# Kernel optimization log

Measured on AMD Instinct MI355X. Metric: run time of the kernel, lower is better.

## Reference

```python
import jax, jax.numpy as jnp
import numpy as np


def setup_inputs() -> dict:
    key = jax.random.key(0)
    ks = jax.random.split(key, 8)
    B, C, H, W = 4, 256, 64, 64
    Ci = C // 8  # inter_channels = 32
    x = jax.random.normal(ks[0], (B, C, H, W), dtype=jnp.float32)
    # 1x1 conv weights stored as [out, in] matrices (kernel size 1)
    sq = 1.0 / np.sqrt(C)
    Wq = jax.random.uniform(ks[1], (Ci, C), jnp.float32, -sq, sq)
    bq = jax.random.uniform(ks[2], (Ci,), jnp.float32, -sq, sq)
    Wk = jax.random.uniform(ks[3], (Ci, C), jnp.float32, -sq, sq)
    bk = jax.random.uniform(ks[4], (Ci,), jnp.float32, -sq, sq)
    Wv = jax.random.uniform(ks[5], (C, C), jnp.float32, -sq, sq)
    bv = jax.random.uniform(ks[6], (C,), jnp.float32, -sq, sq)
    # torch initializes gamma to zeros; use a nonzero value so output depends on attention path
    gamma = jnp.array([0.5], dtype=jnp.float32)
    return {"x": x, "Wq": Wq, "bq": bq, "Wk": Wk, "bk": bk, "Wv": Wv, "bv": bv, "gamma": gamma}


def reference(x, Wq, bq, Wk, bk, Wv, bv, gamma):
    B, C, H, W = x.shape
    N = H * W
    xf = x.reshape(B, C, N)                        # [B, C, N]
    # 1x1 convs == channel-mixing matmuls
    q = jnp.einsum('oc,bcn->bon', Wq, xf) + bq[None, :, None]   # [B, Ci, N]
    k = jnp.einsum('oc,bcn->bon', Wk, xf) + bk[None, :, None]   # [B, Ci, N]
    v = jnp.einsum('oc,bcn->bon', Wv, xf) + bv[None, :, None]   # [B, C,  N]
    # energy[b, n, m] = sum_c q[b, c, n] * k[b, c, m]  (no scaling, per DANet)
    energy = jnp.einsum('bcn,bcm->bnm', q, k)      # [B, N, N]
    attention = jax.nn.softmax(energy, axis=-1)    # softmax over keys m
    # out[b, c, n] = sum_m v[b, c, m] * attention[b, n, m]
    out = jnp.einsum('bcm,bnm->bcn', v, attention)
    out = out.reshape(B, C, H, W)
    return gamma[0] * out + x
```

## Files before the change

### kernel.cpp

```cpp
#include <hip/hip_runtime.h>
#include <hip/hip_bf16.h>
#include <math.h>

typedef __bf16 bf16x8 __attribute__((ext_vector_type(8)));
typedef float  floatx4 __attribute__((ext_vector_type(4)));

#define MFMA(a, b, c) __builtin_amdgcn_mfma_f32_16x16x32_bf16((a), (b), (c), 0, 0, 0)

__device__ __forceinline__ unsigned short f2bf(float f) {
  union { float f; unsigned u; } v; v.f = f;
  unsigned r = v.u + 0x7FFFu + ((v.u >> 16) & 1u);
  return (unsigned short)(r >> 16);
}
__device__ __forceinline__ float bf2f(unsigned short u) {
  union { unsigned u; float f; } v; v.u = ((unsigned)u) << 16;
  return v.f;
}

__global__ __launch_bounds__(256) void k_wconv(const float* __restrict__ Wq,
                                               const float* __restrict__ Wk,
                                               const float* __restrict__ Wv,
                                               unsigned short* __restrict__ Wall) {
  int i = blockIdx.x * 256 + threadIdx.x;
  int o = i >> 8, c = i & 255;
  float v = (o < 32) ? Wq[o * 256 + c]
          : (o < 64) ? Wk[(o - 32) * 256 + c]
                     : Wv[(o - 64) * 256 + c];
  Wall[i] = f2bf(v);
}

__global__ __launch_bounds__(256) void k_xpose(const float* __restrict__ x,
                                               unsigned short* __restrict__ xT) {
  int bid = blockIdx.x;
  int b = bid >> 8, rem = bid & 255;
  int nb = rem >> 2, cb = rem & 3;
  int n0 = nb * 64, c0 = cb * 64;
  int tid = threadIdx.x;
  __shared__ alignas(16) unsigned short T[64][72];
#pragma unroll
  for (int i = 0; i < 4; ++i) {
    int idx = tid + 256 * i;
    int r = idx >> 4, g = idx & 15;
    float4 d = *(const float4*)(x + ((size_t)b * 256 + c0 + r) * 4096 + n0 + g * 4);
    T[g * 4 + 0][r] = f2bf(d.x);
    T[g * 4 + 1][r] = f2bf(d.y);
    T[g * 4 + 2][r] = f2bf(d.z);
    T[g * 4 + 3][r] = f2bf(d.w);
  }
  __syncthreads();
#pragma unroll
  for (int i = 0; i < 2; ++i) {
    int idx = tid + 256 * i;
    int j = idx >> 3, g = idx & 7;
    *(uint4*)(xT + ((size_t)b * 4096 + n0 + j) * 256 + c0 + g * 8) =
        *(const uint4*)&T[j][g * 8];
  }
}

__global__ __launch_bounds__(64, 4) void k_proj(const unsigned short* __restrict__ xT,
                                                const unsigned short* __restrict__ Wall,
                                                const float* __restrict__ bq,
                                                const float* __restrict__ bk,
                                                const float* __restrict__ bv,
                                                unsigned short* __restrict__ qkT,
                                                unsigned short* __restrict__ vbf) {
  int b = blockIdx.x >> 9;
  int m0 = ((blockIdx.x >> 1) & 255) * 16;
  int h = blockIdx.x & 1;
  int lane = threadIdx.x & 63;
  int l15 = lane & 15, quad = lane >> 4;

  floatx4 acc[10];
#pragma unroll
  for (int tt = 0; tt < 10; ++tt) acc[tt] = floatx4{0.f, 0.f, 0.f, 0.f};

  const unsigned short* arow = xT + ((size_t)b * 4096 + m0 + l15) * 256;
#pragma unroll
  for (int ks = 0; ks < 8; ++ks) {
    bf16x8 a = *(const bf16x8*)(arow + ks * 32 + quad * 8);
#pragma unroll
    for (int tt = 0; tt < 10; ++tt) {
      int gt = (tt < 2) ? (h * 2 + tt) : (4 + h * 8 + (tt - 2));
      bf16x8 w = *(const bf16x8*)(Wall + (size_t)(gt * 16 + l15) * 256 + ks * 32 + quad * 8);
      acc[tt] = MFMA(a, w, acc[tt]);
    }
  }
#pragma unroll
  for (int tt = 0; tt < 2; ++tt) {
    int o = (h * 2 + tt) * 16 + l15;
    float bias = (o < 32) ? bq[o] : bk[o - 32];
#pragma unroll
    for (int r = 0; r < 4; ++r) {
      int m = m0 + quad * 4 + r;
      qkT[((size_t)b * 4096 + m) * 64 + o] = f2bf(acc[tt][r] + bias);
    }
  }
  __shared__ alignas(16) unsigned short Os[128][24];
#pragma unroll
  for (int tt = 2; tt < 10; ++tt) {
    int lr = (tt - 2) * 16 + l15;
    int c = h * 128 + lr;
    float bias = bv[c];
#pragma unroll
    for (int r = 0; r < 4; ++r)
      Os[lr][quad * 4 + r] = f2bf(acc[tt][r] + bias);
  }
  __syncthreads();
#pragma unroll
  for (int i = 0; i < 4; ++i) {
    int idx = threadIdx.x + 64 * i;
    int r = idx >> 1, g = idx & 1;
    int c = h * 128 + r;
    *(uint4*)(vbf + ((size_t)b * 256 + c) * 4096 + m0 + g * 8) = *(const uint4*)&Os[r][g * 8];
  }
}

__global__ __launch_bounds__(256, 3) void k_attn(const unsigned short* __restrict__ qkT,
                                                 const unsigned short* __restrict__ vbf,
                                                 unsigned short* __restrict__ Obf,
                                                 float* __restrict__ lsum) {
  const int b = blockIdx.x >> 8;
  const int s = (blockIdx.x >> 6) & 3;
  const int q0 = (blockIdx.x & 63) * 64;
  const int tid = threadIdx.x;
  const int wave = tid >> 6, lane = tid & 63;
  const int l15 = lane & 15, quad = lane >> 4;

  __shared__ alignas(16) unsigned short Kl[2][64][40];
  __shared__ alignas(16) unsigned short Pl[4][16][72];

  bf16x8 aq = *(const bf16x8*)(qkT + ((size_t)b * 4096 + q0 + wave * 16 + l15) * 64 + quad * 8);

  floatx4 O[4][4];
#pragma unroll
  for (int qt = 0; qt < 4; ++qt)
#pragma unroll
    for (int nt = 0; nt < 4; ++nt) O[qt][nt] = floatx4{0.f, 0.f, 0.f, 0.f};

  float l_part = 0.f;
  const floatx4 zero4 = {0.f, 0.f, 0.f, 0.f};

  const unsigned short* vrow = vbf + ((size_t)b * 256 + wave * 64) * 4096;

  {
    int r = tid >> 2, g = tid & 3;
    uint4 d = *(const uint4*)(qkT + ((size_t)b * 4096 + s * 1024 + r) * 64 + 32 + g * 8);
    *(uint4*)&Kl[0][r][g * 8] = d;
  }
  __syncthreads();

  for (int it = 0; it < 16; ++it) {
    const int m0 = (s * 16 + it) * 64;
    const int buf = it & 1;

    bf16x8 vb[4][2];
#pragma unroll
    for (int nt = 0; nt < 4; ++nt)
#pragma unroll
      for (int kk = 0; kk < 2; ++kk)
        vb[nt][kk] = *(const bf16x8*)(vrow + (size_t)(nt * 16 + l15) * 4096 + m0 + kk * 32 + quad * 8);

    floatx4 st[4];
#pragma unroll
    for (int t = 0; t < 4; ++t) {
      bf16x8 kb = *(const bf16x8*)&Kl[buf][t * 16 + l15][quad * 8];
      st[t] = MFMA(kb, aq, zero4);
    }
#pragma unroll
    for (int t = 0; t < 4; ++t) {
      float p0 = __expf(st[t][0]);
      float p1 = __expf(st[t][1]);
      float p2 = __expf(st[t][2]);
      float p3 = __expf(st[t][3]);
      l_part += (p0 + p1) + (p2 + p3);
      ushort4 pk = make_ushort4(f2bf(p0), f2bf(p1), f2bf(p2), f2bf(p3));
      *(ushort4*)&Pl[wave][l15][t * 16 + quad * 4] = pk;
    }

    if (it < 15) {
      int r = tid >> 2, g = tid & 3;
      uint4 d = *(const uint4*)(qkT + ((size_t)b * 4096 + m0 + 64 + r) * 64 + 32 + g * 8);
      *(uint4*)&Kl[buf ^ 1][r][g * 8] = d;
    }
    __syncthreads();

#pragma unroll
    for (int qt = 0; qt < 4; ++qt) {
      bf16x8 pa0 = *(const bf16x8*)&Pl[qt][l15][quad * 8];
      bf16x8 pa1 = *(const bf16x8*)&Pl[qt][l15][32 + quad * 8];
#pragma unroll
      for (int nt = 0; nt < 4; ++nt) {
        O[qt][nt] = MFMA(pa0, vb[nt][0], O[qt][nt]);
        O[qt][nt] = MFMA(pa1, vb[nt][1], O[qt][nt]);
      }
    }
    __syncthreads();
  }

  float lt = l_part;
  lt += __shfl_xor(lt, 16);
  lt += __shfl_xor(lt, 32);
  if (quad == 0)
    lsum[((size_t)s * 4 + b) * 4096 + q0 + wave * 16 + l15] = lt;

#pragma unroll
  for (int nt = 0; nt < 4; ++nt) {
    size_t crow = (((size_t)s * 4 + b) * 256 + wave * 64 + nt * 16 + l15) * 4096;
#pragma unroll
    for (int qt = 0; qt < 4; ++qt) {
      ushort4 ok = make_ushort4(f2bf(O[qt][nt][0]), f2bf(O[qt][nt][1]),
                                f2bf(O[qt][nt][2]), f2bf(O[qt][nt][3]));
      *(ushort4*)(Obf + crow + q0 + qt * 16 + quad * 4) = ok;
    }
  }
}

__global__ __launch_bounds__(256) void k_merge(const unsigned short* __restrict__ Obf,
                                               const float* __restrict__ lsum,
                                               const float* __restrict__ x,
                                               const float* __restrict__ gma,
                                               float* __restrict__ out) {
  int t = blockIdx.x * 256 + threadIdx.x;
  int n4 = t & 1023;
  int c = (t >> 10) & 255;
  int b = t >> 18;
  int n = n4 << 2;
  size_t xa = (((size_t)b * 256 + c) << 12) + n;
  float4 xv = *(const float4*)(x + xa);
  float L0 = 0.f, L1 = 0.f, L2 = 0.f, L3 = 0.f;
  float o0 = 0.f, o1 = 0.f, o2 = 0.f, o3 = 0.f;
#pragma unroll
  for (int s = 0; s < 4; ++s) {
    float4 ls = *(const float4*)(lsum + (((size_t)s * 4 + b) << 12) + n);
    L0 += ls.x; L1 += ls.y; L2 += ls.z; L3 += ls.w;
    ushort4 ov = *(const ushort4*)(Obf + ((((size_t)s * 4 + b) * 256 + c) << 12) + n);
    o0 += bf2f(ov.x); o1 += bf2f(ov.y); o2 += bf2f(ov.z); o3 += bf2f(ov.w);
  }
  float g = gma[0];
  float4 r;
  r.x = xv.x + g * o0 / L0;
  r.y = xv.y + g * o1 / L1;
  r.z = xv.z + g * o2 / L2;
  r.w = xv.w + g * o3 / L3;
  *(float4*)(out + xa) = r;
}

extern "C" void kernel_launch(void* const* d_in, const int* in_sizes, int n_in,
                              void* d_out, int out_size, void* d_ws, size_t ws_size,
                              hipStream_t stream) {
  const float* x   = (const float*)d_in[0];
  const float* Wq  = (const float*)d_in[1];
  const float* bq  = (const float*)d_in[2];
  const float* Wk  = (const float*)d_in[3];
  const float* bk  = (const float*)d_in[4];
  const float* Wv  = (const float*)d_in[5];
  const float* bv  = (const float*)d_in[6];
  const float* gma = (const float*)d_in[7];
  float* out = (float*)d_out;

  unsigned short* qkT  = (unsigned short*)d_ws;
  unsigned short* vbf  = qkT + (size_t)4 * 4096 * 64;
  unsigned short* Wall = vbf + (size_t)4 * 256 * 4096;
  unsigned short* xT   = Wall + (size_t)320 * 256;
  unsigned short* Obf  = xT;
  float* lsum = (float*)(Obf + (size_t)4 * 4 * 256 * 4096);

  k_wconv<<<320, 256, 0, stream>>>(Wq, Wk, Wv, Wall);
  k_xpose<<<1024, 256, 0, stream>>>(x, xT);
  k_proj<<<2048, 64, 0, stream>>>(xT, Wall, bq, bk, bv, qkT, vbf);
  k_attn<<<1024, 256, 0, stream>>>(qkT, vbf, Obf, lsum);
  k_merge<<<4096, 256, 0, stream>>>(Obf, lsum, x, gma, out);
}
```

Before: 191.9 us.

## Fuse transpose into projection and double-buffer P tile to drop a barrier

Removes the separate transpose kernel: each projection block now loads fp32 x directly, converts and transposes it into shared memory, and computes all 320 output channels for 16 positions instead of splitting across two blocks. In attention, the P tile is double-buffered with a layout that makes the A-operand reads contiguous, so the second per-iteration barrier is removed. Packed bf16 conversion intrinsics replace scalar conversions, and attention occupancy hint is raised to 4. This cuts an intermediate global round-trip and one sync per iteration, at the cost of more accumulator registers in projection and fewer projection blocks.

```diff
diff --git a/kernel.cpp b/kernel.cpp
--- a/kernel.cpp
+++ b/kernel.cpp
@@ -15,6 +15,11 @@
 __device__ __forceinline__ float bf2f(unsigned short u) {
   union { unsigned u; float f; } v; v.u = ((unsigned)u) << 16;
   return v.f;
+}
+__device__ __forceinline__ unsigned pk2bf(float a, float b) {
+  __hip_bfloat162 h = __float22bfloat162_rn(make_float2(a, b));
+  union { __hip_bfloat162 h; unsigned u; } v; v.h = h;
+  return v.u;
 }
 
 __global__ __launch_bounds__(256) void k_wconv(const float* __restrict__ Wq,
@@ -29,65 +34,53 @@
   Wall[i] = f2bf(v);
 }
 
-__global__ __launch_bounds__(256) void k_xpose(const float* __restrict__ x,
-                                               unsigned short* __restrict__ xT) {
-  int bid = blockIdx.x;
-  int b = bid >> 8, rem = bid & 255;
-  int nb = rem >> 2, cb = rem & 3;
-  int n0 = nb * 64, c0 = cb * 64;
-  int tid = threadIdx.x;
-  __shared__ alignas(16) unsigned short T[64][72];
-#pragma unroll
-  for (int i = 0; i < 4; ++i) {
-    int idx = tid + 256 * i;
-    int r = idx >> 4, g = idx & 15;
-    float4 d = *(const float4*)(x + ((size_t)b * 256 + c0 + r) * 4096 + n0 + g * 4);
-    T[g * 4 + 0][r] = f2bf(d.x);
-    T[g * 4 + 1][r] = f2bf(d.y);
-    T[g * 4 + 2][r] = f2bf(d.z);
-    T[g * 4 + 3][r] = f2bf(d.w);
-  }
-  __syncthreads();
-#pragma unroll
-  for (int i = 0; i < 2; ++i) {
-    int idx = tid + 256 * i;
-    int j = idx >> 3, g = idx & 7;
-    *(uint4*)(xT + ((size_t)b * 4096 + n0 + j) * 256 + c0 + g * 8) =
-        *(const uint4*)&T[j][g * 8];
-  }
-}
-
-__global__ __launch_bounds__(64, 4) void k_proj(const unsigned short* __restrict__ xT,
+__global__ __launch_bounds__(64, 3) void k_proj(const float* __restrict__ x,
                                                 const unsigned short* __restrict__ Wall,
                                                 const float* __restrict__ bq,
                                                 const float* __restrict__ bk,
                                                 const float* __restrict__ bv,
                                                 unsigned short* __restrict__ qkT,
                                                 unsigned short* __restrict__ vbf) {
-  int b = blockIdx.x >> 9;
-  int m0 = ((blockIdx.x >> 1) & 255) * 16;
-  int h = blockIdx.x & 1;
-  int lane = threadIdx.x & 63;
+  int b = blockIdx.x >> 8;
+  int m0 = (blockIdx.x & 255) * 16;
+  int lane = threadIdx.x;
   int l15 = lane & 15, quad = lane >> 4;
 
-  floatx4 acc[10];
-#pragma unroll
-  for (int tt = 0; tt < 10; ++tt) acc[tt] = floatx4{0.f, 0.f, 0.f, 0.f};
-
-  const unsigned short* arow = xT + ((size_t)b * 4096 + m0 + l15) * 256;
+  __shared__ alignas(16) union {
+    unsigned short T[16][264];
+    unsigned short Os[256][24];
+  } sm;
+
+  const float* xb = x + (size_t)b * 256 * 4096 + m0;
+#pragma unroll
+  for (int i = 0; i < 8; ++i) {
+    int idx = i * 64 + lane;
+    int cp = idx >> 2, nq = idx & 3;
+    float4 fa = *(const float4*)(xb + (size_t)(2 * cp) * 4096 + nq * 4);
+    float4 fb = *(const float4*)(xb + (size_t)(2 * cp + 1) * 4096 + nq * 4);
+    *(unsigned*)&sm.T[nq * 4 + 0][2 * cp] = pk2bf(fa.x, fb.x);
+    *(unsigned*)&sm.T[nq * 4 + 1][2 * cp] = pk2bf(fa.y, fb.y);
+    *(unsigned*)&sm.T[nq * 4 + 2][2 * cp] = pk2bf(fa.z, fb.z);
+    *(unsigned*)&sm.T[nq * 4 + 3][2 * cp] = pk2bf(fa.w, fb.w);
+  }
+  __syncthreads();
+
+  floatx4 acc[20];
+#pragma unroll
+  for (int tt = 0; tt < 20; ++tt) acc[tt] = floatx4{0.f, 0.f, 0.f, 0.f};
+
 #pragma unroll
   for (int ks = 0; ks < 8; ++ks) {
-    bf16x8 a = *(const bf16x8*)(arow + ks * 32 + quad * 8);
-#pragma unroll
-    for (int tt = 0; tt < 10; ++tt) {
-      int gt = (tt < 2) ? (h * 2 + tt) : (4 + h * 8 + (tt - 2));
-      bf16x8 w = *(const bf16x8*)(Wall + (size_t)(gt * 16 + l15) * 256 + ks * 32 + quad * 8);
+    bf16x8 a = *(const bf16x8*)&sm.T[l15][ks * 32 + quad * 8];
+#pragma unroll
+    for (int tt = 0; tt < 20; ++tt) {
+      bf16x8 w = *(const bf16x8*)(Wall + (size_t)(tt * 16 + l15) * 256 + ks * 32 + quad * 8);
       acc[tt] = MFMA(a, w, acc[tt]);
     }
   }
 #pragma unroll
-  for (int tt = 0; tt < 2; ++tt) {
-    int o = (h * 2 + tt) * 16 + l15;
+  for (int tt = 0; tt < 4; ++tt) {
+    int o = tt * 16 + l15;
     float bias = (o < 32) ? bq[o] : bk[o - 32];
 #pragma unroll
     for (int r = 0; r < 4; ++r) {
@@ -95,27 +88,25 @@
       qkT[((size_t)b * 4096 + m) * 64 + o] = f2bf(acc[tt][r] + bias);
     }
   }
-  __shared__ alignas(16) unsigned short Os[128][24];
-#pragma unroll
-  for (int tt = 2; tt < 10; ++tt) {
-    int lr = (tt - 2) * 16 + l15;
-    int c = h * 128 + lr;
+  __syncthreads();
+#pragma unroll
+  for (int tt = 4; tt < 20; ++tt) {
+    int c = (tt - 4) * 16 + l15;
     float bias = bv[c];
 #pragma unroll
     for (int r = 0; r < 4; ++r)
-      Os[lr][quad * 4 + r] = f2bf(acc[tt][r] + bias);
-  }
-  __syncthreads();
-#pragma unroll
-  for (int i = 0; i < 4; ++i) {
-    int idx = threadIdx.x + 64 * i;
+      sm.Os[c][quad * 4 + r] = f2bf(acc[tt][r] + bias);
+  }
+  __syncthreads();
+#pragma unroll
+  for (int i = 0; i < 8; ++i) {
+    int idx = lane + 64 * i;
     int r = idx >> 1, g = idx & 1;
-    int c = h * 128 + r;
-    *(uint4*)(vbf + ((size_t)b * 256 + c) * 4096 + m0 + g * 8) = *(const uint4*)&Os[r][g * 8];
-  }
-}
-
-__global__ __launch_bounds__(256, 3) void k_attn(const unsigned short* __restrict__ qkT,
+    *(uint4*)(vbf + ((size_t)b * 256 + r) * 4096 + m0 + g * 8) = *(const uint4*)&sm.Os[r][g * 8];
+  }
+}
+
+__global__ __launch_bounds__(256, 4) void k_attn(const unsigned short* __restrict__ qkT,
                                                  const unsigned short* __restrict__ vbf,
                                                  unsigned short* __restrict__ Obf,
                                                  float* __restrict__ lsum) {
@@ -127,9 +118,10 @@
   const int l15 = lane & 15, quad = lane >> 4;
 
   __shared__ alignas(16) unsigned short Kl[2][64][40];
-  __shared__ alignas(16) unsigned short Pl[4][16][72];
-
-  bf16x8 aq = *(const bf16x8*)(qkT + ((size_t)b * 4096 + q0 + wave * 16 + l15) * 64 + quad * 8);
+  __shared__ alignas(16) unsigned short Pl[2][4][8][16][8];
+
+  const unsigned short* qbase = qkT + (size_t)b * 4096 * 64;
+  bf16x8 aq = *(const bf16x8*)(qbase + (size_t)(q0 + wave * 16 + l15) * 64 + quad * 8);
 
   floatx4 O[4][4];
 #pragma unroll
@@ -144,10 +136,12 @@
 
   {
     int r = tid >> 2, g = tid & 3;
-    uint4 d = *(const uint4*)(qkT + ((size_t)b * 4096 + s * 1024 + r) * 64 + 32 + g * 8);
+    uint4 d = *(const uint4*)(qbase + (size_t)(s * 1024 + r) * 64 + 32 + g * 8);
     *(uint4*)&Kl[0][r][g * 8] = d;
   }
   __syncthreads();
+
+  const int kc_hi = quad >> 1, kc_lo = (quad & 1) * 4;
 
   for (int it = 0; it < 16; ++it) {
     const int m0 = (s * 16 + it) * 64;
@@ -160,57 +154,51 @@
       for (int kk = 0; kk < 2; ++kk)
         vb[nt][kk] = *(const bf16x8*)(vrow + (size_t)(nt * 16 + l15) * 4096 + m0 + kk * 32 + quad * 8);
 
-    floatx4 st[4];
 #pragma unroll
     for (int t = 0; t < 4; ++t) {
       bf16x8 kb = *(const bf16x8*)&Kl[buf][t * 16 + l15][quad * 8];
-      st[t] = MFMA(kb, aq, zero4);
-    }
-#pragma unroll
-    for (int t = 0; t < 4; ++t) {
-      float p0 = __expf(st[t][0]);
-      float p1 = __expf(st[t][1]);
-      float p2 = __expf(st[t][2]);
-      float p3 = __expf(st[t][3]);
+      floatx4 st = MFMA(kb, aq, zero4);
+      float p0 = __expf(st[0]);
+      float p1 = __expf(st[1]);
+      float p2 = __expf(st[2]);
+      float p3 = __expf(st[3]);
       l_part += (p0 + p1) + (p2 + p3);
-      ushort4 pk = make_ushort4(f2bf(p0), f2bf(p1), f2bf(p2), f2bf(p3));
-      *(ushort4*)&Pl[wave][l15][t * 16 + quad * 4] = pk;
+      uint2 pk = make_uint2(pk2bf(p0, p1), pk2bf(p2, p3));
+      *(uint2*)&Pl[buf][wave][2 * t + kc_hi][l15][kc_lo] = pk;
     }
 
     if (it < 15) {
       int r = tid >> 2, g = tid & 3;
-      uint4 d = *(const uint4*)(qkT + ((size_t)b * 4096 + m0 + 64 + r) * 64 + 32 + g * 8);
+      uint4 d = *(const uint4*)(qbase + (size_t)(m0 + 64 + r) * 64 + 32 + g * 8);
       *(uint4*)&Kl[buf ^ 1][r][g * 8] = d;
     }
     __syncthreads();
 
 #pragma unroll
     for (int qt = 0; qt < 4; ++qt) {
-      bf16x8 pa0 = *(const bf16x8*)&Pl[qt][l15][quad * 8];
-      bf16x8 pa1 = *(const bf16x8*)&Pl[qt][l15][32 + quad * 8];
+      bf16x8 pa0 = *(const bf16x8*)&Pl[buf][qt][quad][l15][0];
+      bf16x8 pa1 = *(const bf16x8*)&Pl[buf][qt][quad + 4][l15][0];
 #pragma unroll
       for (int nt = 0; nt < 4; ++nt) {
         O[qt][nt] = MFMA(pa0, vb[nt][0], O[qt][nt]);
         O[qt][nt] = MFMA(pa1, vb[nt][1], O[qt][nt]);
       }
     }
-    __syncthreads();
-  }
-
-  float lt = l_part;
-  lt += __shfl_xor(lt, 16);
-  lt += __shfl_xor(lt, 32);
+  }
+
+  l_part += __shfl_xor(l_part, 16);
+  l_part += __shfl_xor(l_part, 32);
   if (quad == 0)
-    lsum[((size_t)s * 4 + b) * 4096 + q0 + wave * 16 + l15] = lt;
+    lsum[((size_t)s * 4 + b) * 4096 + q0 + wave * 16 + l15] = l_part;
 
 #pragma unroll
   for (int nt = 0; nt < 4; ++nt) {
     size_t crow = (((size_t)s * 4 + b) * 256 + wave * 64 + nt * 16 + l15) * 4096;
 #pragma unroll
     for (int qt = 0; qt < 4; ++qt) {
-      ushort4 ok = make_ushort4(f2bf(O[qt][nt][0]), f2bf(O[qt][nt][1]),
-                                f2bf(O[qt][nt][2]), f2bf(O[qt][nt][3]));
-      *(ushort4*)(Obf + crow + q0 + qt * 16 + quad * 4) = ok;
+      uint2 ok = make_uint2(pk2bf(O[qt][nt][0], O[qt][nt][1]),
+                            pk2bf(O[qt][nt][2], O[qt][nt][3]));
+      *(uint2*)(Obf + crow + q0 + qt * 16 + quad * 4) = ok;
     }
   }
 }
@@ -261,13 +249,11 @@
   unsigned short* qkT  = (unsigned short*)d_ws;
   unsigned short* vbf  = qkT + (size_t)4 * 4096 * 64;
   unsigned short* Wall = vbf + (size_t)4 * 256 * 4096;
-  unsigned short* xT   = Wall + (size_t)320 * 256;
-  unsigned short* Obf  = xT;
+  unsigned short* Obf  = Wall + (size_t)320 * 256;
   float* lsum = (float*)(Obf + (size_t)4 * 4 * 256 * 4096);
 
   k_wconv<<<320, 256, 0, stream>>>(Wq, Wk, Wv, Wall);
-  k_xpose<<<1024, 256, 0, stream>>>(x, xT);
-  k_proj<<<2048, 64, 0, stream>>>(xT, Wall, bq, bk, bv, qkT, vbf);
+  k_proj<<<1024, 64, 0, stream>>>(x, Wall, bq, bk, bv, qkT, vbf);
   k_attn<<<1024, 256, 0, stream>>>(qkT, vbf, Obf, lsum);
   k_merge<<<4096, 256, 0, stream>>>(Obf, lsum, x, gma, out);
 }
```

Measured after the change: 195.1 us. No clear change (+1.7%).
